# Kernel tuning notes

Hardware: AMD Instinct MI355X
Metric: run time of the kernel (lower is better)

The kernel has to match this reference:

```python
import jax, jax.numpy as jnp
import numpy as np

B, C, H, W = 64, 512, 8, 8
K = 100            # num_class
H1, HID, L = 64, 128, 32   # ae_hidden[0], fixed hidd, ae_latent
CLIP = 100.0       # CSSRClassifier.clip_len
RED = -0.1         # model='pcssr' -> -1, times gamma=0.1
PUSH_THRESH = 10000.0


def setup_inputs() -> dict:
    key = jax.random.key(0)
    ks = jax.random.split(key, 9)
    s = lambda fan_in: 1.0 / np.sqrt(fan_in)  # kaiming-ish 1x1 conv init scale
    return {
        "x": jax.random.normal(ks[0], (B, C, H, W), jnp.float32),
        "ycls": jax.random.randint(ks[1], (B,), 0, K),
        "safe_margin_all": jax.random.normal(ks[2], (K,), jnp.float32),
        "safe_distance_all": jax.random.normal(ks[3], (K,), jnp.float32),
        "W1": jax.random.normal(ks[4], (K, H1, C), jnp.float32) * s(C),
        "W2": jax.random.normal(ks[5], (K, HID, H1), jnp.float32) * s(H1),
        "W3": jax.random.normal(ks[6], (K, L, HID), jnp.float32) * s(HID),
        "prototypes": jax.random.normal(ks[7], (K, L, H, W), jnp.float32),
        "prototypes1": jax.random.normal(ks[8], (K, L, H, W), jnp.float32),
    }


def reference(x, ycls, safe_margin_all, safe_distance_all, W1, W2, W3, prototypes, prototypes1):
    P = H * W
    xf = x.reshape(B, C, P)
    # per-class 1x1-conv encoder (tanh after every conv), batched over classes k
    h = jnp.tanh(jnp.einsum('koc,bcp->kbop', W1, xf))      # [K,B,H1,P]
    h = jnp.tanh(jnp.einsum('koi,kbip->kbop', W2, h))      # [K,B,HID,P]
    lt = jnp.tanh(jnp.einsum('koi,kbip->kbop', W3, h))     # [K,B,L,P]
    p = prototypes.reshape(K, 1, L, P)
    p1 = prototypes1.reshape(K, 1, L, P)
    # squared-L2 distance over channel dim, scaled by reduction, clipped
    er = jnp.clip(jnp.sum((lt - p) ** 2, axis=2) * RED, -CLIP, CLIP)    # [K,B,P]
    er1 = jnp.clip(jnp.sum((lt - p1) ** 2, axis=2) * RED, -CLIP, CLIP)  # [K,B,P]
    # training losses (pull on er1, push on er), vectorized across classes
    f = jnp.sum(er, axis=2)    # [K,B] spatial-summed errors
    f1 = jnp.sum(er1, axis=2)  # [K,B]
    cls_ids = jnp.arange(K)[:, None]
    mask_eq = (ycls[None, :] == cls_ids).astype(f.dtype)   # [K,B]
    n_eq = jnp.sum(mask_eq, axis=1)
    pull = jnp.sum(jnp.where(n_eq > 0,
                             jnp.sum(f1 * mask_eq, axis=1) / jnp.maximum(n_eq, 1.0),
                             0.0))
    comb = (1.0 - mask_eq) * (f < PUSH_THRESH).astype(f.dtype)
    n_comb = jnp.sum(comb, axis=1)
    push = jnp.sum(jnp.where(n_comb > 0,
                             jnp.sum(f * comb, axis=1) / jnp.maximum(n_comb, 1.0),
                             0.0))
    # cat per-class [B,1,H,W] errors along dim 1 -> [B,K,H,W]
    logits = jnp.transpose(er, (1, 0, 2)).reshape(B, K, H, W)
    logits1 = jnp.transpose(er1, (1, 0, 2)).reshape(B, K, H, W)
    return logits, logits1, pull, push
```

## Files before the change

### kernel.cpp

```cpp
#include <hip/hip_runtime.h>

typedef short  s16x8  __attribute__((ext_vector_type(8)));
typedef float  f32x16 __attribute__((ext_vector_type(16)));
typedef unsigned short u16;
typedef unsigned long long u64b;

#define MFMA32(a,b,c) __builtin_amdgcn_mfma_f32_32x32x16_bf16((a),(b),(c),0,0,0)
#define KCLS 100

__device__ __forceinline__ u16 f2bf(float f) {
  return (u16)(__builtin_bit_cast(unsigned, f) >> 16);
}

__device__ __forceinline__ unsigned pk2(float lo, float hi) {
  return __builtin_amdgcn_perm(__builtin_bit_cast(unsigned, hi),
                               __builtin_bit_cast(unsigned, lo), 0x07060302u);
}
__device__ __forceinline__ u64b pk4(float v0, float v1, float v2, float v3) {
  return (u64b)pk2(v0, v1) | ((u64b)pk2(v2, v3) << 32);
}

__device__ __forceinline__ float tanh_fast(float x) {
  float e = __builtin_amdgcn_exp2f(x * 2.8853900817779268f);
  return 1.0f - 2.0f * __builtin_amdgcn_rcpf(e + 1.0f);
}

__device__ __forceinline__ void ld_lds16(const void* g, void* l) {
  __builtin_amdgcn_global_load_lds(
      (const __attribute__((address_space(1))) unsigned char*)g,
      (__attribute__((address_space(3))) unsigned char*)l, 16, 0, 0);
}

__global__ void prep(const float* __restrict__ x, const float* __restrict__ w1,
                     const float* __restrict__ w2, const float* __restrict__ w3,
                     u16* __restrict__ xF, u16* __restrict__ W1F,
                     u16* __restrict__ W2F, u16* __restrict__ W3F,
                     float* __restrict__ fz, float* __restrict__ out2) {
  __shared__ float tile[64][65];
  const int bid = blockIdx.x, t = threadIdx.x;
  if (bid == 0 && t < 2) out2[t] = 0.f;
  if (bid < 512) {
    const int b = bid >> 3, ck = bid & 7;
    #pragma unroll
    for (int j = 0; j < 4; j++) {
      int e4 = j * 1024 + t * 4;
      int c = e4 >> 6, p0 = e4 & 63;
      float4 v = *(const float4*)(x + ((size_t)b * 512 + ck * 64 + c) * 64 + p0);
      tile[c][p0] = v.x; tile[c][p0 + 1] = v.y; tile[c][p0 + 2] = v.z; tile[c][p0 + 3] = v.w;
    }
    __syncthreads();
    #pragma unroll
    for (int i = 0; i < 2; i++) {
      int s = i * 256 + t;
      int ksl = s >> 7, ph = (s >> 6) & 1, lane = s & 63;
      int cb = ksl * 16 + (lane >> 5) * 8, pp = ph * 32 + (lane & 31);
      u16 o[8];
      #pragma unroll
      for (int jj = 0; jj < 8; jj++) o[jj] = f2bf(tile[cb + jj][pp]);
      *(uint4*)(xF + (((size_t)b * 64 + (ck * 4 + ksl) * 2 + ph) * 512) + lane * 8) = *(uint4*)o;
    }
  } else if (bid < 1312) {
    int base = (bid - 512) * 512;
    #pragma unroll
    for (int i = 0; i < 2; i++) {
      int s = base + i * 256 + t;
      int frag = s >> 6, lane = s & 63;
      int k = frag >> 6, fr = frag & 63;
      int m = (fr & 1) * 32 + (lane & 31);
      int c0 = (fr >> 1) * 16 + (lane >> 5) * 8;
      const float* src = w1 + ((size_t)k * 64 + m) * 512 + c0;
      float4 a = *(const float4*)src, b4 = *(const float4*)(src + 4);
      u16 o[8] = { f2bf(a.x), f2bf(a.y), f2bf(a.z), f2bf(a.w),
                   f2bf(b4.x), f2bf(b4.y), f2bf(b4.z), f2bf(b4.w) };
      *(uint4*)(W1F + ((size_t)frag * 512) + lane * 8) = *(uint4*)o;
    }
  } else if (bid < 1512) {
    int base = (bid - 1312) * 512;
    #pragma unroll
    for (int i = 0; i < 2; i++) {
      int s = base + i * 256 + t;
      int frag = s >> 6, lane = s & 63;
      int k = frag >> 4, fr = frag & 15;
      int m = (fr & 3) * 32 + (lane & 31);
      int c0 = (fr >> 2) * 16 + (lane >> 5) * 8;
      const float* src = w2 + ((size_t)k * 128 + m) * 64 + c0;
      float4 a = *(const float4*)src, b4 = *(const float4*)(src + 4);
      u16 o[8] = { f2bf(a.x), f2bf(a.y), f2bf(a.z), f2bf(a.w),
                   f2bf(b4.x), f2bf(b4.y), f2bf(b4.z), f2bf(b4.w) };
      *(uint4*)(W2F + ((size_t)frag * 512) + lane * 8) = *(uint4*)o;
    }
  } else if (bid < 1612) {
    int base = (bid - 1512) * 512;
    #pragma unroll
    for (int i = 0; i < 2; i++) {
      int s = base + i * 256 + t;
      int frag = s >> 6, lane = s & 63;
      int k = frag >> 3, kb = frag & 7;
      int m = lane & 31;
      int c0 = kb * 16 + (lane >> 5) * 8;
      const float* src = w3 + ((size_t)k * 32 + m) * 128 + c0;
      float4 a = *(const float4*)src, b4 = *(const float4*)(src + 4);
      u16 o[8] = { f2bf(a.x), f2bf(a.y), f2bf(a.z), f2bf(a.w),
                   f2bf(b4.x), f2bf(b4.y), f2bf(b4.z), f2bf(b4.w) };
      *(uint4*)(W3F + ((size_t)frag * 512) + lane * 8) = *(uint4*)o;
    }
  } else {
    int i4 = (bid - 1612) * 256 + t;
    if (i4 < 3200) {
      float4 z = {0.f, 0.f, 0.f, 0.f};
      *(float4*)(fz + (size_t)i4 * 4) = z;
    }
  }
}

__global__ __launch_bounds__(256, 2) void cssr_main(
    const u16* __restrict__ W1F, const u16* __restrict__ W2F, const u16* __restrict__ W3F,
    const u16* __restrict__ xF, const float* __restrict__ protos,
    const float* __restrict__ protos1, float* __restrict__ out,
    float* __restrict__ fw, float* __restrict__ f1w)
{
  __shared__ u16 pool[40960];

  const int bid = blockIdx.x;
  const int kp = bid >> 6, b = bid & 63;
  const int tid = threadIdx.x, w = tid >> 6, lane = tid & 63;
  const int nhalf = lane >> 5, nn = lane & 31;
  const int kk = w >> 1, mt = w & 1;
  const int k = kp * 2 + kk;

  const u16* xb = xF + ((size_t)b * 64) * 512;

  #pragma unroll
  for (int i = 0; i < 16; i++) {
    int f = w * 16 + i;
    ld_lds16(xb + (size_t)f * 512 + lane * 8, &pool[f * 512]);
  }
  __syncthreads();

  f32x16 acc1[2] = {};
  #pragma unroll 8
  for (int g = 0; g < 32; g++) {
    s16x8 A = *(const s16x8*)(W1F + (((size_t)k * 64 + g * 2 + mt) * 512) + lane * 8);
    #pragma unroll
    for (int nt = 0; nt < 2; nt++) {
      s16x8 B = *(const s16x8*)&pool[(g * 2 + nt) * 512 + lane * 8];
      acc1[nt] = MFMA32(A, B, acc1[nt]);
    }
  }

  #pragma unroll
  for (int nt = 0; nt < 2; nt++) {
    #pragma unroll
    for (int g = 0; g < 4; g++) {
      u64b hv = pk4(tanh_fast(acc1[nt][g * 4 + 0]), tanh_fast(acc1[nt][g * 4 + 1]),
                    tanh_fast(acc1[nt][g * 4 + 2]), tanh_fast(acc1[nt][g * 4 + 3]));
      int kb = mt * 2 + (g >> 1);
      int tl = (g & 1) * 32 + nn;
      *(u64b*)&pool[32768 + kk * 4096 + (kb * 2 + nt) * 512 + tl * 8 + nhalf * 4] = hv;
    }
  }
  __syncthreads();

  f32x16 acc2[2][2] = {};
  #pragma unroll
  for (int kb = 0; kb < 4; kb++) {
    s16x8 A0 = *(const s16x8*)(W2F + (((size_t)k * 16 + kb * 4 + mt * 2 + 0) * 512) + lane * 8);
    s16x8 A1 = *(const s16x8*)(W2F + (((size_t)k * 16 + kb * 4 + mt * 2 + 1) * 512) + lane * 8);
    #pragma unroll
    for (int nh = 0; nh < 2; nh++) {
      s16x8 B = *(const s16x8*)&pool[32768 + kk * 4096 + (kb * 2 + nh) * 512 + lane * 8];
      acc2[0][nh] = MFMA32(A0, B, acc2[0][nh]);
      acc2[1][nh] = MFMA32(A1, B, acc2[1][nh]);
    }
  }
  #pragma unroll
  for (int m4l = 0; m4l < 2; m4l++) {
    #pragma unroll
    for (int nh = 0; nh < 2; nh++) {
      #pragma unroll
      for (int g = 0; g < 4; g++) {
        u64b hv = pk4(tanh_fast(acc2[m4l][nh][g * 4 + 0]), tanh_fast(acc2[m4l][nh][g * 4 + 1]),
                      tanh_fast(acc2[m4l][nh][g * 4 + 2]), tanh_fast(acc2[m4l][nh][g * 4 + 3]));
        int kb2 = mt * 4 + m4l * 2 + (g >> 1);
        int tl  = (g & 1) * 32 + nn;
        *(u64b*)&pool[kk * 8192 + (kb2 * 2 + nh) * 512 + tl * 8 + nhalf * 4] = hv;
      }
    }
  }
  __syncthreads();

  f32x16 acc3 = {};
  #pragma unroll
  for (int kb = 0; kb < 8; kb++) {
    s16x8 A = *(const s16x8*)(W3F + (((size_t)k * 8 + kb) * 512) + lane * 8);
    s16x8 B = *(const s16x8*)&pool[kk * 8192 + (kb * 2 + mt) * 512 + lane * 8];
    acc3 = MFMA32(A, B, acc3);
  }

  const int p = mt * 32 + nn;
  const float* pr  = protos  + (size_t)k * 2048;
  const float* pr1 = protos1 + (size_t)k * 2048;
  float d2 = 0.f, d21 = 0.f;
  #pragma unroll
  for (int g = 0; g < 4; g++) {
    #pragma unroll
    for (int q = 0; q < 4; q++) {
      int m = q + 8 * g + 4 * nhalf;
      float lt = tanh_fast(acc3[g * 4 + q]);
      float d = lt - pr [m * 64 + p];  d2  += d * d;
      float e = lt - pr1[m * 64 + p];  d21 += e * e;
    }
  }
  d2 += __shfl_xor(d2, 32); d21 += __shfl_xor(d21, 32);
  float er  = fminf(fmaxf(d2  * -0.1f, -100.f), 100.f);
  float er1 = fminf(fmaxf(d21 * -0.1f, -100.f), 100.f);
  if (nhalf == 0) {
    out[(size_t)b * 6400 + k * 64 + p]          = er;
    out[409600 + (size_t)b * 6400 + k * 64 + p] = er1;
  }
  float s = er, s1 = er1;
  s += __shfl_xor(s, 1);  s1 += __shfl_xor(s1, 1);
  s += __shfl_xor(s, 2);  s1 += __shfl_xor(s1, 2);
  s += __shfl_xor(s, 4);  s1 += __shfl_xor(s1, 4);
  s += __shfl_xor(s, 8);  s1 += __shfl_xor(s1, 8);
  s += __shfl_xor(s, 16); s1 += __shfl_xor(s1, 16);
  if (lane == 0) {
    atomicAdd(&fw [k * 64 + b], s);
    atomicAdd(&f1w[k * 64 + b], s1);
  }
}

__global__ void finalize(const float* __restrict__ f, const float* __restrict__ f1,
                         const int* __restrict__ ycls, float* __restrict__ out2) {
  const int k = blockIdx.x, b = threadIdx.x;
  float fv = f[k * 64 + b], f1v = f1[k * 64 + b];
  bool eq = (ycls[b] == k);
  bool cb = (!eq) && (fv < 10000.f);
  float s1 = eq ? f1v : 0.f, ne = eq ? 1.f : 0.f;
  float s  = cb ? fv  : 0.f, nc = cb ? 1.f : 0.f;
  #pragma unroll
  for (int o = 1; o < 64; o <<= 1) {
    s1 += __shfl_xor(s1, o); ne += __shfl_xor(ne, o);
    s  += __shfl_xor(s,  o); nc += __shfl_xor(nc, o);
  }
  if (b == 0) {
    if (ne > 0.f) atomicAdd(&out2[0], s1 / ne);
    if (nc > 0.f) atomicAdd(&out2[1], s / nc);
  }
}

extern "C" void kernel_launch(void* const* d_in, const int* in_sizes, int n_in,
                              void* d_out, int out_size, void* d_ws, size_t ws_size,
                              hipStream_t stream) {
  const float* x     = (const float*)d_in[0];
  const int*   ycls  = (const int*)d_in[1];
  const float* W1    = (const float*)d_in[4];
  const float* W2    = (const float*)d_in[5];
  const float* W3    = (const float*)d_in[6];
  const float* prot  = (const float*)d_in[7];
  const float* prot1 = (const float*)d_in[8];
  float* out = (float*)d_out;

  char* ws = (char*)d_ws;
  u16*  xFb = (u16*)(ws);
  u16*  W1F = (u16*)(ws + 4194304);
  u16*  W2F = (u16*)(ws + 10747904);
  u16*  W3F = (u16*)(ws + 12386304);
  float* fw  = (float*)(ws + 13205504);
  float* f1w = (float*)(ws + 13231104);

  prep<<<1625, 256, 0, stream>>>(x, W1, W2, W3, xFb, W1F, W2F, W3F,
                                 fw, out + 819200);
  cssr_main<<<50 * 64, 256, 0, stream>>>(W1F, W2F, W3F, xFb, prot, prot1,
                                         out, fw, f1w);
  finalize<<<KCLS, 64, 0, stream>>>(fw, f1w, ycls, out + 819200);
}
```

Measured before the change: 173.0 us.

## Add producer wave double-buffering x tiles and shrink LDS for occupancy

Adds a fifth wave per block that streams the x tile into LDS in four double-buffered chunks while the four compute waves run the first-layer MFMAs on the previous chunk. LDS use drops from 80KB to 32KB and launch bounds go to 320 threads with a higher target occupancy, so more blocks can share a CU. The cost is extra barriers per chunk, one wave idle during the later layers, and tighter register limits that could cause spills.

```diff
diff --git a/kernel.cpp b/kernel.cpp
--- a/kernel.cpp
+++ b/kernel.cpp
@@ -7,6 +7,9 @@
 
 #define MFMA32(a,b,c) __builtin_amdgcn_mfma_f32_32x32x16_bf16((a),(b),(c),0,0,0)
 #define KCLS 100
+
+#define WAIT_VM0   0x0F70
+#define WAIT_LGKM0 0xC07F
 
 __device__ __forceinline__ u16 f2bf(float f) {
   return (u16)(__builtin_bit_cast(unsigned, f) >> 16);
@@ -113,120 +116,146 @@
   }
 }
 
-__global__ __launch_bounds__(256, 2) void cssr_main(
+__global__ __launch_bounds__(320, 6) void cssr_main(
     const u16* __restrict__ W1F, const u16* __restrict__ W2F, const u16* __restrict__ W3F,
     const u16* __restrict__ xF, const float* __restrict__ protos,
     const float* __restrict__ protos1, float* __restrict__ out,
     float* __restrict__ fw, float* __restrict__ f1w)
 {
-  __shared__ u16 pool[40960];
+  __shared__ u16 pool[16384];
 
   const int bid = blockIdx.x;
   const int kp = bid >> 6, b = bid & 63;
   const int tid = threadIdx.x, w = tid >> 6, lane = tid & 63;
   const int nhalf = lane >> 5, nn = lane & 31;
   const int kk = w >> 1, mt = w & 1;
-  const int k = kp * 2 + kk;
+  const int k = kp * 2 + (kk & 1);
 
   const u16* xb = xF + ((size_t)b * 64) * 512;
 
-  #pragma unroll
-  for (int i = 0; i < 16; i++) {
-    int f = w * 16 + i;
-    ld_lds16(xb + (size_t)f * 512 + lane * 8, &pool[f * 512]);
+  f32x16 acc1[2] = {};
+  if (w == 4) {
+    #pragma unroll
+    for (int i = 0; i < 16; i++)
+      ld_lds16(xb + (size_t)i * 512 + lane * 8, &pool[i * 512]);
+    __builtin_amdgcn_s_waitcnt(WAIT_VM0);
+  }
+  __builtin_amdgcn_s_barrier();
+
+  for (int ci = 0; ci < 4; ci++) {
+    const int pb = ci & 1;
+    if (w == 4) {
+      if (ci < 3) {
+        #pragma unroll
+        for (int i = 0; i < 16; i++)
+          ld_lds16(xb + (size_t)((ci + 1) * 16 + i) * 512 + lane * 8,
+                   &pool[(pb ^ 1) * 8192 + i * 512]);
+        __builtin_amdgcn_s_waitcnt(WAIT_VM0);
+      }
+    } else {
+      #pragma unroll
+      for (int ksl = 0; ksl < 8; ksl++) {
+        s16x8 A = *(const s16x8*)(W1F + (((size_t)k * 64 + (ci * 8 + ksl) * 2 + mt) * 512) + lane * 8);
+        #pragma unroll
+        for (int nt = 0; nt < 2; nt++) {
+          s16x8 B = *(const s16x8*)&pool[pb * 8192 + (ksl * 2 + nt) * 512 + lane * 8];
+          acc1[nt] = MFMA32(A, B, acc1[nt]);
+        }
+      }
+      __builtin_amdgcn_s_waitcnt(WAIT_LGKM0);
+    }
+    __builtin_amdgcn_s_barrier();
+  }
+
+  if (w < 4) {
+    #pragma unroll
+    for (int nt = 0; nt < 2; nt++) {
+      #pragma unroll
+      for (int g = 0; g < 4; g++) {
+        u64b hv = pk4(tanh_fast(acc1[nt][g * 4 + 0]), tanh_fast(acc1[nt][g * 4 + 1]),
+                      tanh_fast(acc1[nt][g * 4 + 2]), tanh_fast(acc1[nt][g * 4 + 3]));
+        int kb = mt * 2 + (g >> 1);
+        int tl = (g & 1) * 32 + nn;
+        *(u64b*)&pool[kk * 4096 + (kb * 2 + nt) * 512 + tl * 8 + nhalf * 4] = hv;
+      }
+    }
   }
   __syncthreads();
 
-  f32x16 acc1[2] = {};
-  #pragma unroll 8
-  for (int g = 0; g < 32; g++) {
-    s16x8 A = *(const s16x8*)(W1F + (((size_t)k * 64 + g * 2 + mt) * 512) + lane * 8);
-    #pragma unroll
-    for (int nt = 0; nt < 2; nt++) {
-      s16x8 B = *(const s16x8*)&pool[(g * 2 + nt) * 512 + lane * 8];
-      acc1[nt] = MFMA32(A, B, acc1[nt]);
-    }
-  }
-
-  #pragma unroll
-  for (int nt = 0; nt < 2; nt++) {
+  f32x16 acc2[2][2] = {};
+  if (w < 4) {
+    #pragma unroll
+    for (int kb = 0; kb < 4; kb++) {
+      s16x8 A0 = *(const s16x8*)(W2F + (((size_t)k * 16 + kb * 4 + mt * 2 + 0) * 512) + lane * 8);
+      s16x8 A1 = *(const s16x8*)(W2F + (((size_t)k * 16 + kb * 4 + mt * 2 + 1) * 512) + lane * 8);
+      #pragma unroll
+      for (int nh = 0; nh < 2; nh++) {
+        s16x8 B = *(const s16x8*)&pool[kk * 4096 + (kb * 2 + nh) * 512 + lane * 8];
+        acc2[0][nh] = MFMA32(A0, B, acc2[0][nh]);
+        acc2[1][nh] = MFMA32(A1, B, acc2[1][nh]);
+      }
+    }
+  }
+  __syncthreads();
+
+  if (w < 4) {
+    #pragma unroll
+    for (int m4l = 0; m4l < 2; m4l++) {
+      #pragma unroll
+      for (int nh = 0; nh < 2; nh++) {
+        #pragma unroll
+        for (int g = 0; g < 4; g++) {
+          u64b hv = pk4(tanh_fast(acc2[m4l][nh][g * 4 + 0]), tanh_fast(acc2[m4l][nh][g * 4 + 1]),
+                        tanh_fast(acc2[m4l][nh][g * 4 + 2]), tanh_fast(acc2[m4l][nh][g * 4 + 3]));
+          int kb2 = mt * 4 + m4l * 2 + (g >> 1);
+          int tl  = (g & 1) * 32 + nn;
+          *(u64b*)&pool[kk * 8192 + (kb2 * 2 + nh) * 512 + tl * 8 + nhalf * 4] = hv;
+        }
+      }
+    }
+  }
+  __syncthreads();
+
+  if (w < 4) {
+    f32x16 acc3 = {};
+    #pragma unroll
+    for (int kb = 0; kb < 8; kb++) {
+      s16x8 A = *(const s16x8*)(W3F + (((size_t)k * 8 + kb) * 512) + lane * 8);
+      s16x8 B = *(const s16x8*)&pool[kk * 8192 + (kb * 2 + mt) * 512 + lane * 8];
+      acc3 = MFMA32(A, B, acc3);
+    }
+
+    const int p = mt * 32 + nn;
+    const float* pr  = protos  + (size_t)k * 2048;
+    const float* pr1 = protos1 + (size_t)k * 2048;
+    float d2 = 0.f, d21 = 0.f;
     #pragma unroll
     for (int g = 0; g < 4; g++) {
-      u64b hv = pk4(tanh_fast(acc1[nt][g * 4 + 0]), tanh_fast(acc1[nt][g * 4 + 1]),
-                    tanh_fast(acc1[nt][g * 4 + 2]), tanh_fast(acc1[nt][g * 4 + 3]));
-      int kb = mt * 2 + (g >> 1);
-      int tl = (g & 1) * 32 + nn;
-      *(u64b*)&pool[32768 + kk * 4096 + (kb * 2 + nt) * 512 + tl * 8 + nhalf * 4] = hv;
-    }
-  }
-  __syncthreads();
-
-  f32x16 acc2[2][2] = {};
-  #pragma unroll
-  for (int kb = 0; kb < 4; kb++) {
-    s16x8 A0 = *(const s16x8*)(W2F + (((size_t)k * 16 + kb * 4 + mt * 2 + 0) * 512) + lane * 8);
-    s16x8 A1 = *(const s16x8*)(W2F + (((size_t)k * 16 + kb * 4 + mt * 2 + 1) * 512) + lane * 8);
-    #pragma unroll
-    for (int nh = 0; nh < 2; nh++) {
-      s16x8 B = *(const s16x8*)&pool[32768 + kk * 4096 + (kb * 2 + nh) * 512 + lane * 8];
-      acc2[0][nh] = MFMA32(A0, B, acc2[0][nh]);
-      acc2[1][nh] = MFMA32(A1, B, acc2[1][nh]);
-    }
-  }
-  #pragma unroll
-  for (int m4l = 0; m4l < 2; m4l++) {
-    #pragma unroll
-    for (int nh = 0; nh < 2; nh++) {
-      #pragma unroll
-      for (int g = 0; g < 4; g++) {
-        u64b hv = pk4(tanh_fast(acc2[m4l][nh][g * 4 + 0]), tanh_fast(acc2[m4l][nh][g * 4 + 1]),
-                      tanh_fast(acc2[m4l][nh][g * 4 + 2]), tanh_fast(acc2[m4l][nh][g * 4 + 3]));
-        int kb2 = mt * 4 + m4l * 2 + (g >> 1);
-        int tl  = (g & 1) * 32 + nn;
-        *(u64b*)&pool[kk * 8192 + (kb2 * 2 + nh) * 512 + tl * 8 + nhalf * 4] = hv;
-      }
-    }
-  }
-  __syncthreads();
-
-  f32x16 acc3 = {};
-  #pragma unroll
-  for (int kb = 0; kb < 8; kb++) {
-    s16x8 A = *(const s16x8*)(W3F + (((size_t)k * 8 + kb) * 512) + lane * 8);
-    s16x8 B = *(const s16x8*)&pool[kk * 8192 + (kb * 2 + mt) * 512 + lane * 8];
-    acc3 = MFMA32(A, B, acc3);
-  }
-
-  const int p = mt * 32 + nn;
-  const float* pr  = protos  + (size_t)k * 2048;
-  const float* pr1 = protos1 + (size_t)k * 2048;
-  float d2 = 0.f, d21 = 0.f;
-  #pragma unroll
-  for (int g = 0; g < 4; g++) {
-    #pragma unroll
-    for (int q = 0; q < 4; q++) {
-      int m = q + 8 * g + 4 * nhalf;
-      float lt = tanh_fast(acc3[g * 4 + q]);
-      float d = lt - pr [m * 64 + p];  d2  += d * d;
-      float e = lt - pr1[m * 64 + p];  d21 += e * e;
-    }
-  }
-  d2 += __shfl_xor(d2, 32); d21 += __shfl_xor(d21, 32);
-  float er  = fminf(fmaxf(d2  * -0.1f, -100.f), 100.f);
-  float er1 = fminf(fmaxf(d21 * -0.1f, -100.f), 100.f);
-  if (nhalf == 0) {
-    out[(size_t)b * 6400 + k * 64 + p]          = er;
-    out[409600 + (size_t)b * 6400 + k * 64 + p] = er1;
-  }
-  float s = er, s1 = er1;
-  s += __shfl_xor(s, 1);  s1 += __shfl_xor(s1, 1);
-  s += __shfl_xor(s, 2);  s1 += __shfl_xor(s1, 2);
-  s += __shfl_xor(s, 4);  s1 += __shfl_xor(s1, 4);
-  s += __shfl_xor(s, 8);  s1 += __shfl_xor(s1, 8);
-  s += __shfl_xor(s, 16); s1 += __shfl_xor(s1, 16);
-  if (lane == 0) {
-    atomicAdd(&fw [k * 64 + b], s);
-    atomicAdd(&f1w[k * 64 + b], s1);
+      #pragma unroll
+      for (int q = 0; q < 4; q++) {
+        int m = q + 8 * g + 4 * nhalf;
+        float lt = tanh_fast(acc3[g * 4 + q]);
+        float d = lt - pr [m * 64 + p];  d2  += d * d;
+        float e = lt - pr1[m * 64 + p];  d21 += e * e;
+      }
+    }
+    d2 += __shfl_xor(d2, 32); d21 += __shfl_xor(d21, 32);
+    float er  = fminf(fmaxf(d2  * -0.1f, -100.f), 100.f);
+    float er1 = fminf(fmaxf(d21 * -0.1f, -100.f), 100.f);
+    if (nhalf == 0) {
+      out[(size_t)b * 6400 + k * 64 + p]          = er;
+      out[409600 + (size_t)b * 6400 + k * 64 + p] = er1;
+    }
+    float s = er, s1 = er1;
+    s += __shfl_xor(s, 1);  s1 += __shfl_xor(s1, 1);
+    s += __shfl_xor(s, 2);  s1 += __shfl_xor(s1, 2);
+    s += __shfl_xor(s, 4);  s1 += __shfl_xor(s1, 4);
+    s += __shfl_xor(s, 8);  s1 += __shfl_xor(s1, 8);
+    s += __shfl_xor(s, 16); s1 += __shfl_xor(s1, 16);
+    if (lane == 0) {
+      atomicAdd(&fw [k * 64 + b], s);
+      atomicAdd(&f1w[k * 64 + b], s1);
+    }
   }
 }
 
@@ -271,7 +300,7 @@
 
   prep<<<1625, 256, 0, stream>>>(x, W1, W2, W3, xFb, W1F, W2F, W3F,
                                  fw, out + 819200);
-  cssr_main<<<50 * 64, 256, 0, stream>>>(W1F, W2F, W3F, xFb, prot, prot1,
+  cssr_main<<<50 * 64, 320, 0, stream>>>(W1F, W2F, W3F, xFb, prot, prot1,
                                          out, fw, f1w);
   finalize<<<KCLS, 64, 0, stream>>>(fw, f1w, ycls, out + 819200);
 }
```

New measurement: 201.1 us. +16.2%, slower.
